# Optimization experiments

Hardware: AMD Instinct MI355X
Metric: run time of the kernel (lower is better)

Reference implementation:

```python
import jax, jax.numpy as jnp
import numpy as np

# Hyperparameters mirroring init_kwargs
MAX_ITERS = 100      # ADMM outer iterations
RHO = 1.0            # ADMM penalty
INNER = 20           # PGD steps per x-subproblem
STEP = 5e-05         # fixed PGD step (x_inner_step given, so no svdvals branch)


def setup_inputs() -> dict:
    key = jax.random.key(0)
    kA, kb, kc = jax.random.split(key, 3)
    m, n = 2048, 4096
    A = jax.random.normal(kA, (m, n), dtype=jnp.float32)
    b = jax.random.uniform(kb, (m,), dtype=jnp.float32)
    c = jax.random.uniform(kc, (n,), dtype=jnp.float32)
    return {"A": A, "b": b, "c": c}


def _admm(A, b, c):
    m, n = A.shape

    def outer(carry, _):
        x, s, u = carry
        r = s + b - u  # target for the x-subproblem residual

        # PGD on: min_{x>=0} c^T x + (rho/2)||A x - r||^2
        def pgd(x, _):
            g = c + RHO * (A.T @ (A @ x - r))
            return jnp.maximum(x - STEP * g, 0.0), None

        x, _ = jax.lax.scan(pgd, x, None, length=INNER)

        Ax = A @ x
        s = jnp.maximum(Ax - b + u, 0.0)   # slack update (projection onto >=0)
        u = u + (Ax - s - b)               # scaled dual update
        return (x, s, u), None

    init = (jnp.zeros((n,), A.dtype), jnp.zeros((m,), A.dtype), jnp.zeros((m,), A.dtype))
    (x, s, u), _ = jax.lax.scan(outer, init, None, length=MAX_ITERS)
    lambda_kkt = -RHO * u
    return x, s, u, lambda_kkt


def reference(A, b, c):
    # return_history=False -> torch module returns (x, s, u, lambda_kkt, None);
    # we return the 4 tensor outputs.
    return _admm(A, b, c)
```

## Files before the change

kernel.cpp:

```cpp
#include <hip/hip_runtime.h>
#include <hip/hip_cooperative_groups.h>

namespace cg = cooperative_groups;

#define M_ROWS 2048
#define N_COLS 4096
#define RHO_C 1.0f
#define STEP_C 5e-05f
#define MAX_ITERS_C 100
#define INNER_C 20

__device__ __forceinline__ unsigned long long ald64(const unsigned long long* p) {
    return __hip_atomic_load(p, __ATOMIC_RELAXED, __HIP_MEMORY_SCOPE_AGENT);
}
__device__ __forceinline__ void ast64(unsigned long long* p, unsigned long long v) {
    __hip_atomic_store(p, v, __ATOMIC_RELAXED, __HIP_MEMORY_SCOPE_AGENT);
}
__device__ __forceinline__ unsigned long long packf(float f, unsigned tag) {
    union { float f; unsigned u; } c; c.f = f;
    return ((unsigned long long)tag << 32) | (unsigned long long)c.u;
}
__device__ __forceinline__ float unpackf(unsigned long long v) {
    union { unsigned u; float f; } c; c.u = (unsigned)v; return c.f;
}

#define STAGE_X(TAG)                                                         \
    {                                                                        \
        const unsigned long long* xp =                                       \
            xP + ((((unsigned)(TAG)) & 1u) << 12) + ((unsigned)tid << 2);    \
        unsigned long long w0, w1, w2, w3;                                   \
        for (;;) {                                                           \
            w0 = ald64(xp + 0); w1 = ald64(xp + 1);                          \
            w2 = ald64(xp + 2); w3 = ald64(xp + 3);                          \
            unsigned mm = ((unsigned)(w0 >> 32) ^ (unsigned)(TAG))           \
                        | ((unsigned)(w1 >> 32) ^ (unsigned)(TAG))           \
                        | ((unsigned)(w2 >> 32) ^ (unsigned)(TAG))           \
                        | ((unsigned)(w3 >> 32) ^ (unsigned)(TAG));          \
            if (mm == 0u) break;                                             \
            __builtin_amdgcn_s_sleep(1);                                     \
        }                                                                    \
        xs4[tid] = make_float4(unpackf(w0), unpackf(w1),                     \
                               unpackf(w2), unpackf(w3));                    \
    }                                                                        \
    __syncthreads();

__global__ __launch_bounds__(1024) void admm_df(
    const float* __restrict__ A, const float* __restrict__ bvec,
    const float* __restrict__ cvec, float* __restrict__ out,
    unsigned long long* __restrict__ xP,
    unsigned long long* __restrict__ rtP)
{
    cg::grid_group grid = cg::this_grid();
    const int tid  = threadIdx.x;
    const int blk  = blockIdx.x;
    const int lane = tid & 63;
    const int wave = tid >> 6;
    const int cgp  = wave >> 2;
    const int rq   = wave & 3;

    __shared__ float  abuf[4 * N_COLS];
    __shared__ float4 xs4[1024];
    __shared__ float  red[4][16];
    __shared__ float4 gred[64];
    __shared__ float  wl[16], cw[16];
    __shared__ float  sv[8], uv[8], tpart[16];

    float* xs = reinterpret_cast<float*>(xs4);
    const float4* A4 = reinterpret_cast<const float4*>(A);
    float4* abuf4 = reinterpret_cast<float4*>(abuf);

    if (tid < 16) {
        cw[tid] = cvec[blk * 16 + tid];
        ast64(&xP[blk * 16 + tid],        packf(0.0f, 0u));
        ast64(&xP[4096 + blk * 16 + tid], packf(0.0f, 0xFFFFFFFFu));
    }
    if (tid < 8) {
        sv[tid] = 0.0f; uv[tid] = 0.0f;
        ast64(&rtP[blk * 8 + tid], packf(bvec[blk * 8 + tid], 0u));
    }

    float accM[4][16];
    #pragma unroll
    for (int r = 0; r < 4; ++r)
        #pragma unroll
        for (int k = 0; k < 16; ++k) accM[r][k] = 0.0f;

    for (int i0 = 0; i0 < M_ROWS; i0 += 4) {
        #pragma unroll
        for (int ii = 0; ii < 4; ++ii)
            abuf4[ii * 1024 + tid] = A4[(size_t)(i0 + ii) * 1024 + tid];
        __syncthreads();
        #pragma unroll
        for (int ii = 0; ii < 4; ++ii) {
            const float*  row  = abuf + ii * N_COLS;
            const float4* row4 = abuf4 + ii * 1024;
            float4 av[4];
            #pragma unroll
            for (int q = 0; q < 4; ++q)
                av[q] = row4[256 * cgp + 64 * q + lane];
            float cb[4];
            #pragma unroll
            for (int r = 0; r < 4; ++r) cb[r] = row[blk * 16 + rq * 4 + r];
            #pragma unroll
            for (int r = 0; r < 4; ++r)
                #pragma unroll
                for (int q = 0; q < 4; ++q) {
                    accM[r][4 * q + 0] = fmaf(cb[r], av[q].x, accM[r][4 * q + 0]);
                    accM[r][4 * q + 1] = fmaf(cb[r], av[q].y, accM[r][4 * q + 1]);
                    accM[r][4 * q + 2] = fmaf(cb[r], av[q].z, accM[r][4 * q + 2]);
                    accM[r][4 * q + 3] = fmaf(cb[r], av[q].w, accM[r][4 * q + 3]);
                }
        }
        __syncthreads();
    }

    grid.sync();

    unsigned t = 0;
    STAGE_X(0u)

    for (int outer = 0; outer < MAX_ITERS_C; ++outer) {
        {
            const unsigned long long* rp = rtP + tid;
            unsigned long long wa, wb;
            for (;;) {
                wa = ald64(rp); wb = ald64(rp + 1024);
                unsigned mm = ((unsigned)(wa >> 32) ^ (unsigned)outer)
                            | ((unsigned)(wb >> 32) ^ (unsigned)outer);
                if (mm == 0u) break;
                __builtin_amdgcn_s_sleep(1);
            }
            abuf[tid]        = unpackf(wa);
            abuf[tid + 1024] = unpackf(wb);
        }
        __syncthreads();
        {
            const int p = tid >> 2, gq = tid & 3;
            float4 acc = {0.f, 0.f, 0.f, 0.f};
            #pragma unroll
            for (int k2 = 0; k2 < 8; ++k2) {
                const int i = p + 256 * k2;
                const float tv = abuf[i];
                float4 a = A4[(size_t)i * 1024 + blk * 4 + gq];
                acc.x = fmaf(a.x, tv, acc.x); acc.y = fmaf(a.y, tv, acc.y);
                acc.z = fmaf(a.z, tv, acc.z); acc.w = fmaf(a.w, tv, acc.w);
            }
            #pragma unroll
            for (int off = 4; off < 64; off <<= 1) {
                acc.x += __shfl_xor(acc.x, off);
                acc.y += __shfl_xor(acc.y, off);
                acc.z += __shfl_xor(acc.z, off);
                acc.w += __shfl_xor(acc.w, off);
            }
            if ((lane >> 2) == 0) gred[wave * 4 + gq] = acc;
        }
        __syncthreads();
        if (tid < 4) {
            float4 tot = {0.f, 0.f, 0.f, 0.f};
            #pragma unroll
            for (int w = 0; w < 16; ++w) {
                float4 v = gred[w * 4 + tid];
                tot.x += v.x; tot.y += v.y; tot.z += v.z; tot.w += v.w;
            }
            wl[tid * 4 + 0] = tot.x; wl[tid * 4 + 1] = tot.y;
            wl[tid * 4 + 2] = tot.z; wl[tid * 4 + 3] = tot.w;
        }
        __syncthreads();

        for (int inner = 0; inner < INNER_C; ++inner) {
            if (inner != 0) { STAGE_X(t) }

            float4 xq[4];
            #pragma unroll
            for (int q = 0; q < 4; ++q)
                xq[q] = xs4[256 * cgp + 64 * q + lane];

            float4 pd = {0.f, 0.f, 0.f, 0.f};
            #pragma unroll
            for (int q = 0; q < 4; ++q) {
                pd.x = fmaf(accM[0][4*q+0], xq[q].x, pd.x);
                pd.x = fmaf(accM[0][4*q+1], xq[q].y, pd.x);
                pd.x = fmaf(accM[0][4*q+2], xq[q].z, pd.x);
                pd.x = fmaf(accM[0][4*q+3], xq[q].w, pd.x);
                pd.y = fmaf(accM[1][4*q+0], xq[q].x, pd.y);
                pd.y = fmaf(accM[1][4*q+1], xq[q].y, pd.y);
                pd.y = fmaf(accM[1][4*q+2], xq[q].z, pd.y);
                pd.y = fmaf(accM[1][4*q+3], xq[q].w, pd.y);
                pd.z = fmaf(accM[2][4*q+0], xq[q].x, pd.z);
                pd.z = fmaf(accM[2][4*q+1], xq[q].y, pd.z);
                pd.z = fmaf(accM[2][4*q+2], xq[q].z, pd.z);
                pd.z = fmaf(accM[2][4*q+3], xq[q].w, pd.z);
                pd.w = fmaf(accM[3][4*q+0], xq[q].x, pd.w);
                pd.w = fmaf(accM[3][4*q+1], xq[q].y, pd.w);
                pd.w = fmaf(accM[3][4*q+2], xq[q].z, pd.w);
                pd.w = fmaf(accM[3][4*q+3], xq[q].w, pd.w);
            }

            #pragma unroll
            for (int off = 32; off; off >>= 1) {
                pd.x += __shfl_xor(pd.x, off);
                pd.y += __shfl_xor(pd.y, off);
                pd.z += __shfl_xor(pd.z, off);
                pd.w += __shfl_xor(pd.w, off);
            }
            if (lane == 0) {
                red[cgp][rq * 4 + 0] = pd.x;
                red[cgp][rq * 4 + 1] = pd.y;
                red[cgp][rq * 4 + 2] = pd.z;
                red[cgp][rq * 4 + 3] = pd.w;
            }
            __syncthreads();

            if (tid < 16) {
                const float y = red[0][tid] + red[1][tid]
                              + red[2][tid] + red[3][tid];
                const float g = cw[tid] + RHO_C * (y - wl[tid]);
                float xn = xs[blk * 16 + tid] - STEP_C * g;
                xn = xn > 0.f ? xn : 0.f;
                ast64(&xP[(((t + 1u) & 1u) << 12) + blk * 16 + tid],
                      packf(xn, t + 1u));
            }
            ++t;
        }

        STAGE_X(t)
        {
            const int r = blk * 8 + (wave >> 1), h = wave & 1;
            const float4* Ar = A4 + (size_t)r * 1024 + h * 512;
            const float4* xh = xs4 + h * 512;
            float4 acc = {0.f, 0.f, 0.f, 0.f};
            #pragma unroll
            for (int it = 0; it < 8; ++it) {
                float4 a = Ar[it * 64 + lane], xv = xh[it * 64 + lane];
                acc.x = fmaf(a.x, xv.x, acc.x); acc.y = fmaf(a.y, xv.y, acc.y);
                acc.z = fmaf(a.z, xv.z, acc.z); acc.w = fmaf(a.w, xv.w, acc.w);
            }
            float d = acc.x + acc.y + acc.z + acc.w;
            #pragma unroll
            for (int off = 32; off; off >>= 1) d += __shfl_xor(d, off);
            if (lane == 0) tpart[wave] = d;
        }
        __syncthreads();
        if (tid < 8) {
            const int i = blk * 8 + tid;
            const float a  = tpart[2 * tid] + tpart[2 * tid + 1];
            const float bb = bvec[i];
            const float uu = uv[tid];
            float sn = a - bb + uu; sn = sn > 0.f ? sn : 0.f;
            const float un = uu + a - sn - bb;
            sv[tid] = sn; uv[tid] = un;
            ast64(&rtP[i], packf(sn + bb - un, (unsigned)outer + 1u));
        }
    }

    if (tid < 16) out[blk * 16 + tid] = xs[blk * 16 + tid];
    if (tid < 8) {
        const int i = blk * 8 + tid;
        out[4096 + i] = sv[tid];
        out[6144 + i] = uv[tid];
        out[8192 + i] = -uv[tid];
    }
}

extern "C" void kernel_launch(void* const* d_in, const int* in_sizes, int n_in,
                              void* d_out, int out_size, void* d_ws, size_t ws_size,
                              hipStream_t stream) {
    const float* A    = (const float*)d_in[0];
    const float* bvec = (const float*)d_in[1];
    const float* cvec = (const float*)d_in[2];
    float* out = (float*)d_out;

    unsigned long long* xP  = (unsigned long long*)d_ws;
    unsigned long long* rtP = xP + 2 * 4096;

    void* args[] = { (void*)&A, (void*)&bvec, (void*)&cvec, (void*)&out,
                     (void*)&xP, (void*)&rtP };
    hipError_t err = hipLaunchCooperativeKernel((const void*)admm_df,
                               dim3(256), dim3(1024), args, 0, stream);
    (void)err;
}
```

Baseline: 12.52 ms.

## Replace per-element tagged values with per-block flags for cross-block exchange

The inter-block exchange of x and the residual target switches from 64-bit words that each carry an iteration tag to packed float pairs plus one release flag per block. Each consumer thread polls a single flag per producer block, then reads two packed values, which halves the exchange payload and removes the per-element tag checks. Each block also skips fetching its own slice and keeps it in shared memory instead. The cost is that a single thread now serializes the 16- and 8-element updates and waits on s_waitcnt before publishing. Ordering relies on relaxed atomics plus that waitcnt rather than on explicit release/acquire semantics, which risks visibility races.

Result: slower. 16.62 ms (+32.8%).

```diff
diff --git a/kernel.cpp b/kernel.cpp
--- a/kernel.cpp
+++ b/kernel.cpp
@@ -16,39 +16,42 @@
 __device__ __forceinline__ void ast64(unsigned long long* p, unsigned long long v) {
     __hip_atomic_store(p, v, __ATOMIC_RELAXED, __HIP_MEMORY_SCOPE_AGENT);
 }
-__device__ __forceinline__ unsigned long long packf(float f, unsigned tag) {
-    union { float f; unsigned u; } c; c.f = f;
-    return ((unsigned long long)tag << 32) | (unsigned long long)c.u;
-}
-__device__ __forceinline__ float unpackf(unsigned long long v) {
-    union { unsigned u; float f; } c; c.u = (unsigned)v; return c.f;
+__device__ __forceinline__ unsigned aldu(const unsigned* p) {
+    return __hip_atomic_load(p, __ATOMIC_RELAXED, __HIP_MEMORY_SCOPE_AGENT);
+}
+__device__ __forceinline__ void astu(unsigned* p, unsigned v) {
+    __hip_atomic_store(p, v, __ATOMIC_RELAXED, __HIP_MEMORY_SCOPE_AGENT);
+}
+__device__ __forceinline__ float2 u2f(unsigned long long v) {
+    union { unsigned long long u; float2 f; } c; c.u = v; return c.f;
+}
+__device__ __forceinline__ unsigned long long f2u(float a, float b) {
+    union { float2 f; unsigned long long u; } c; c.f = make_float2(a, b); return c.u;
 }
 
 #define STAGE_X(TAG)                                                         \
     {                                                                        \
-        const unsigned long long* xp =                                       \
-            xP + ((((unsigned)(TAG)) & 1u) << 12) + ((unsigned)tid << 2);    \
-        unsigned long long w0, w1, w2, w3;                                   \
-        for (;;) {                                                           \
-            w0 = ald64(xp + 0); w1 = ald64(xp + 1);                          \
-            w2 = ald64(xp + 2); w3 = ald64(xp + 3);                          \
-            unsigned mm = ((unsigned)(w0 >> 32) ^ (unsigned)(TAG))           \
-                        | ((unsigned)(w1 >> 32) ^ (unsigned)(TAG))           \
-                        | ((unsigned)(w2 >> 32) ^ (unsigned)(TAG))           \
-                        | ((unsigned)(w3 >> 32) ^ (unsigned)(TAG));          \
-            if (mm == 0u) break;                                             \
-            __builtin_amdgcn_s_sleep(1);                                     \
+        const int pb = tid >> 2;                                             \
+        if (pb != blk) {                                                     \
+            while (aldu(&flagX[pb]) < (unsigned)(TAG))                       \
+                __builtin_amdgcn_s_sleep(1);                                 \
+            asm volatile("" ::: "memory");                                   \
+            const unsigned long long* src =                                  \
+                xL + ((((unsigned)(TAG)) & 1u) ? 2048u : 0u)                 \
+                   + ((unsigned)tid << 1);                                   \
+            float2 a = u2f(ald64(src)), b = u2f(ald64(src + 1));             \
+            xs4[tid] = make_float4(a.x, a.y, b.x, b.y);                      \
         }                                                                    \
-        xs4[tid] = make_float4(unpackf(w0), unpackf(w1),                     \
-                               unpackf(w2), unpackf(w3));                    \
     }                                                                        \
     __syncthreads();
 
-__global__ __launch_bounds__(1024) void admm_df(
+__global__ __launch_bounds__(1024) void admm_flag(
     const float* __restrict__ A, const float* __restrict__ bvec,
     const float* __restrict__ cvec, float* __restrict__ out,
-    unsigned long long* __restrict__ xP,
-    unsigned long long* __restrict__ rtP)
+    unsigned long long* __restrict__ xL,
+    unsigned long long* __restrict__ rtL,
+    unsigned* __restrict__ flagX,
+    unsigned* __restrict__ flagR)
 {
     cg::grid_group grid = cg::this_grid();
     const int tid  = threadIdx.x;
@@ -63,7 +66,7 @@
     __shared__ float  red[4][16];
     __shared__ float4 gred[64];
     __shared__ float  wl[16], cw[16];
-    __shared__ float  sv[8], uv[8], tpart[16];
+    __shared__ float  sv[8], uv[8], bv[8], tpart[16];
 
     float* xs = reinterpret_cast<float*>(xs4);
     const float4* A4 = reinterpret_cast<const float4*>(A);
@@ -71,13 +74,17 @@
 
     if (tid < 16) {
         cw[tid] = cvec[blk * 16 + tid];
-        ast64(&xP[blk * 16 + tid],        packf(0.0f, 0u));
-        ast64(&xP[4096 + blk * 16 + tid], packf(0.0f, 0xFFFFFFFFu));
+        xs[blk * 16 + tid] = 0.0f;
     }
     if (tid < 8) {
         sv[tid] = 0.0f; uv[tid] = 0.0f;
-        ast64(&rtP[blk * 8 + tid], packf(bvec[blk * 8 + tid], 0u));
-    }
+        bv[tid] = bvec[blk * 8 + tid];
+        ast64(xL + blk * 8 + tid, 0ull);
+    }
+    if (tid < 4)
+        ast64(rtL + blk * 4 + tid,
+              f2u(bvec[blk * 8 + 2 * tid], bvec[blk * 8 + 2 * tid + 1]));
+    if (tid == 0) { astu(&flagX[blk], 0u); astu(&flagR[blk], 0u); }
 
     float accM[4][16];
     #pragma unroll
@@ -116,22 +123,22 @@
 
     grid.sync();
 
+    if (tid < 8) abuf[blk * 8 + tid] = bv[tid];
+
     unsigned t = 0;
     STAGE_X(0u)
 
     for (int outer = 0; outer < MAX_ITERS_C; ++outer) {
         {
-            const unsigned long long* rp = rtP + tid;
-            unsigned long long wa, wb;
-            for (;;) {
-                wa = ald64(rp); wb = ald64(rp + 1024);
-                unsigned mm = ((unsigned)(wa >> 32) ^ (unsigned)outer)
-                            | ((unsigned)(wb >> 32) ^ (unsigned)outer);
-                if (mm == 0u) break;
-                __builtin_amdgcn_s_sleep(1);
-            }
-            abuf[tid]        = unpackf(wa);
-            abuf[tid + 1024] = unpackf(wb);
+            const int pb = tid >> 2;
+            if (pb != blk) {
+                while (aldu(&flagR[pb]) < (unsigned)outer)
+                    __builtin_amdgcn_s_sleep(1);
+                asm volatile("" ::: "memory");
+                float2 v = u2f(ald64(rtL + (pb << 2) + (tid & 3)));
+                abuf[(pb << 3) + ((tid & 3) << 1)]     = v.x;
+                abuf[(pb << 3) + ((tid & 3) << 1) + 1] = v.y;
+            }
         }
         __syncthreads();
         {
@@ -211,14 +218,25 @@
             }
             __syncthreads();
 
-            if (tid < 16) {
-                const float y = red[0][tid] + red[1][tid]
-                              + red[2][tid] + red[3][tid];
-                const float g = cw[tid] + RHO_C * (y - wl[tid]);
-                float xn = xs[blk * 16 + tid] - STEP_C * g;
-                xn = xn > 0.f ? xn : 0.f;
-                ast64(&xP[(((t + 1u) & 1u) << 12) + blk * 16 + tid],
-                      packf(xn, t + 1u));
+            if (tid == 0) {
+                float xn[16];
+                #pragma unroll
+                for (int j = 0; j < 16; ++j) {
+                    const float y = red[0][j] + red[1][j]
+                                  + red[2][j] + red[3][j];
+                    const float g = cw[j] + RHO_C * (y - wl[j]);
+                    float v = xs[blk * 16 + j] - STEP_C * g;
+                    xn[j] = v > 0.f ? v : 0.f;
+                }
+                #pragma unroll
+                for (int j = 0; j < 16; ++j) xs[blk * 16 + j] = xn[j];
+                unsigned long long* dst =
+                    xL + (((t + 1u) & 1u) ? 2048u : 0u) + (blk << 3);
+                #pragma unroll
+                for (int j = 0; j < 8; ++j)
+                    ast64(dst + j, f2u(xn[2 * j], xn[2 * j + 1]));
+                asm volatile("s_waitcnt vmcnt(0)" ::: "memory");
+                astu(&flagX[blk], t + 1u);
             }
             ++t;
         }
@@ -241,18 +259,28 @@
             if (lane == 0) tpart[wave] = d;
         }
         __syncthreads();
-        if (tid < 8) {
-            const int i = blk * 8 + tid;
-            const float a  = tpart[2 * tid] + tpart[2 * tid + 1];
-            const float bb = bvec[i];
-            const float uu = uv[tid];
-            float sn = a - bb + uu; sn = sn > 0.f ? sn : 0.f;
-            const float un = uu + a - sn - bb;
-            sv[tid] = sn; uv[tid] = un;
-            ast64(&rtP[i], packf(sn + bb - un, (unsigned)outer + 1u));
-        }
-    }
-
+        if (tid == 0) {
+            float rtv[8];
+            #pragma unroll
+            for (int j = 0; j < 8; ++j) {
+                const float a  = tpart[2 * j] + tpart[2 * j + 1];
+                const float bb = bv[j];
+                const float uu = uv[j];
+                float sn = a - bb + uu; sn = sn > 0.f ? sn : 0.f;
+                const float un = uu + a - sn - bb;
+                sv[j] = sn; uv[j] = un;
+                rtv[j] = sn + bb - un;
+                abuf[blk * 8 + j] = rtv[j];
+            }
+            #pragma unroll
+            for (int j = 0; j < 4; ++j)
+                ast64(rtL + (blk << 2) + j, f2u(rtv[2 * j], rtv[2 * j + 1]));
+            asm volatile("s_waitcnt vmcnt(0)" ::: "memory");
+            astu(&flagR[blk], (unsigned)outer + 1u);
+        }
+    }
+
+    __syncthreads();
     if (tid < 16) out[blk * 16 + tid] = xs[blk * 16 + tid];
     if (tid < 8) {
         const int i = blk * 8 + tid;
@@ -270,12 +298,14 @@
     const float* cvec = (const float*)d_in[2];
     float* out = (float*)d_out;
 
-    unsigned long long* xP  = (unsigned long long*)d_ws;
-    unsigned long long* rtP = xP + 2 * 4096;
+    unsigned long long* xL  = (unsigned long long*)d_ws;
+    unsigned long long* rtL = xL + 2 * 2048;
+    unsigned* flagX = (unsigned*)(rtL + 1024);
+    unsigned* flagR = flagX + 256;
 
     void* args[] = { (void*)&A, (void*)&bvec, (void*)&cvec, (void*)&out,
-                     (void*)&xP, (void*)&rtP };
-    hipError_t err = hipLaunchCooperativeKernel((const void*)admm_df,
+                     (void*)&xL, (void*)&rtL, (void*)&flagX, (void*)&flagR };
+    hipError_t err = hipLaunchCooperativeKernel((const void*)admm_flag,
                                dim3(256), dim3(1024), args, 0, stream);
     (void)err;
 }
```
